# Optimization experiments

Measured on AMD Instinct MI355X. Metric: run time of the kernel, lower is better.

## Reference

```python
import jax, jax.numpy as jnp
import numpy as np

B, H, W, C = 32, 112, 112, 192
KH = KW = 3


def setup_inputs() -> dict:
    key = jax.random.key(0)
    k1, k2 = jax.random.split(key)
    x = jax.random.normal(k1, (B, H, W, C), dtype=jnp.float32)
    # depthwise kernel, HWIO with I=1 and feature_group_count=C (depth_multiplier=1)
    w = jax.random.normal(k2, (KH, KW, 1, C), dtype=jnp.float32) * 0.1
    b = jnp.zeros((C,), dtype=jnp.float32)
    return {"x": x, "w": w, "b": b}


def reference(x, w, b):
    # Depthwise conv = grouped conv with feature_group_count == channels_in.
    # stride 1, 'same' padding, dilation 1, depth_multiplier 1, linear activation.
    out = jax.lax.conv_general_dilated(
        x, w,
        window_strides=(1, 1),
        padding='SAME',
        rhs_dilation=(1, 1),
        dimension_numbers=('NHWC', 'HWIO', 'NHWC'),
        feature_group_count=C,
    )
    return out + b  # bias broadcast over channel axis
```

## Files before the change

kernel.cpp:

```cpp
#include <hip/hip_runtime.h>


constexpr int Bn = 32, Hn = 112, Wn = 112, Cn = 192, C4 = 48;
constexpr int PW = 8, PC = 8;
constexpr int WP = 14, CP = 6, HG = 4;
constexpr int NSTEP = 7;
constexpr int ROWB = 10 * PC * 16;
constexpr int GRPB = 5 * 1024;
constexpr int WLDS = 3 * GRPB;

typedef float floatx4 __attribute__((ext_vector_type(4)));

#define VMWAIT(n) asm volatile("s_waitcnt vmcnt(" #n ")" ::: "memory")

__device__ __forceinline__ floatx4 fma4(floatx4 a, floatx4 b, floatx4 c) {
  c.x = fmaf(a.x, b.x, c.x);
  c.y = fmaf(a.y, b.y, c.y);
  c.z = fmaf(a.z, b.z, c.z);
  c.w = fmaf(a.w, b.w, c.w);
  return c;
}

__global__ __launch_bounds__(128, 2) void dwconv3x3_wavepriv(
    const float* __restrict__ x,
    const float* __restrict__ wgt,
    const float* __restrict__ bias,
    float* __restrict__ out) {
  __shared__ char lds[2 * WLDS];
  const int tid = (int)threadIdx.x;
  const int lane = tid & 63;
  const int wave = tid >> 6;

  int bid = blockIdx.x;
  int chk = gridDim.x >> 3;
  int sbid = (bid & 7) * chk + (bid >> 3);
  int pid = sbid * 2 + wave;
  int cp = pid % CP;  int t1 = pid / CP;
  int wp = t1 % WP;   t1 /= WP;
  int hg = t1 & 3;    int b = t1 >> 2;

  const int hbase = hg * 28;
  const int w0 = wp * PW;
  const float* xb = x + (long)b * Hn * Wn * Cn;
  const int rstr = Wn * Cn;
  char* wl = lds + wave * WLDS;

  int rowadd[5], coloff[5];
#pragma unroll
  for (int k = 0; k < 5; ++k) {
    int q = k * 64 + lane;
    rowadd[k] = q / 80;
    int rem = q % 80;
    int col = rem >> 3, c4 = rem & 7;
    int wc = min(max(w0 + col - 1, 0), Wn - 1);
    coloff[k] = wc * Cn + cp * 32 + c4 * 4;
  }

  auto stage = [&](int g) {
    char* dst0 = wl + (g % 3) * GRPB;
#pragma unroll
    for (int k = 0; k < 5; ++k) {
      int h = min(max(hbase + 4 * g + rowadd[k] - 1, 0), Hn - 1);
      const float* src = xb + (long)h * rstr + coloff[k];
      __builtin_amdgcn_global_load_lds(
          (const __attribute__((address_space(1))) void*)src,
          (__attribute__((address_space(3))) void*)(dst0 + k * 1024),
          16, 0, 0);
    }
  };

  stage(0); stage(1); stage(2);

  const int c4i = lane & 7;
  const int wi = lane >> 3;
  const int cofs = cp * 32 + c4i * 4;
  const int wg = w0 + wi;
  const float cs0 = (wg >= 1) ? 1.f : 0.f;
  const float cs2 = (wg <= Wn - 2) ? 1.f : 0.f;
  floatx4 wv[3][3];
#pragma unroll
  for (int kh = 0; kh < 3; ++kh) {
#pragma unroll
    for (int kw = 0; kw < 3; ++kw)
      wv[kh][kw] = *(const floatx4*)(wgt + (kh * 3 + kw) * Cn + cofs);
    wv[kh][0] *= cs0;
    wv[kh][2] *= cs2;
  }
  const floatx4 bv = *(const floatx4*)(bias + cofs);
  const float sTop = (hg == 0) ? 0.f : 1.f;
  const float sBot = (hg == HG - 1) ? 0.f : 1.f;

  const int ostr = Wn * C4;
  floatx4* outp = (floatx4*)out +
      ((long)(b * Hn + hbase) * Wn + wg) * C4 + cp * PC + c4i;

#pragma unroll
  for (int t = 0; t < NSTEP; ++t) {
    if (t == 0)      VMWAIT(5);
    else if (t == 1) VMWAIT(9);
    else if (t < 6)  VMWAIT(13);
    else             VMWAIT(8);

    floatx4 acc[4];
#pragma unroll
    for (int o = 0; o < 4; ++o) acc[o] = bv;

#pragma unroll
    for (int r = 0; r < 6; ++r) {
      const int s = 4 * t + r;
      const char* base =
          wl + (s >> 2) % 3 * GRPB + (s & 3) * ROWB + 128 + lane * 16;
      floatx4 xv0 = *(const floatx4*)(base - 128);
      floatx4 xv1 = *(const floatx4*)(base);
      floatx4 xv2 = *(const floatx4*)(base + 128);
      if (t == 0 && r == 0) { xv0 *= sTop; xv1 *= sTop; xv2 *= sTop; }
      if (t == NSTEP - 1 && r == 5) { xv0 *= sBot; xv1 *= sBot; xv2 *= sBot; }
#pragma unroll
      for (int kh = 0; kh < 3; ++kh) {
        int o = r - kh;
        if (o >= 0 && o < 4) {
          acc[o] = fma4(xv0, wv[kh][0], acc[o]);
          acc[o] = fma4(xv1, wv[kh][1], acc[o]);
          acc[o] = fma4(xv2, wv[kh][2], acc[o]);
        }
      }
    }

    asm volatile("s_waitcnt lgkmcnt(0)" ::: "memory");
    __builtin_amdgcn_sched_barrier(0);
    if (t <= 4) stage(t + 3);

#pragma unroll
    for (int o = 0; o < 4; ++o)
      __builtin_nontemporal_store(acc[o], outp + (long)(4 * t + o) * ostr);
  }
}

extern "C" void kernel_launch(void* const* d_in, const int* in_sizes, int n_in,
                              void* d_out, int out_size, void* d_ws, size_t ws_size,
                              hipStream_t stream) {
  const float* x = (const float*)d_in[0];
  const float* w = (const float*)d_in[1];
  const float* b = (const float*)d_in[2];
  float* out = (float*)d_out;

  const int grid = Bn * HG * WP * CP / 2;
  dwconv3x3_wavepriv<<<grid, 128, 0, stream>>>(x, w, b, out);
}
```

Measured before the change: 107.8 us.

## Restructure depthwise conv to full-channel width-4 tiles with shared LDS pipeline

Each block of three waves now covers all 192 channels for a 4-column strip over 28 rows. It computes 2 output rows per step, where before each wave privately handled an 8-column, 32-channel patch with 4 rows per step. Rows are staged cooperatively into a 4-slot LDS ring with a block barrier, and the next stage is issued before compute instead of after it. The aim is contiguous full-row channel loads and more resident blocks (launch bounds 192,4). The trade-off is more halo overhead (6 columns loaded per 4 output columns versus 10 per 8), more rows re-read across steps, and a barrier in every step.

```diff
diff --git a/kernel.cpp b/kernel.cpp
--- a/kernel.cpp
+++ b/kernel.cpp
@@ -2,12 +2,14 @@
 
 
 constexpr int Bn = 32, Hn = 112, Wn = 112, Cn = 192, C4 = 48;
-constexpr int PW = 8, PC = 8;
-constexpr int WP = 14, CP = 6, HG = 4;
-constexpr int NSTEP = 7;
-constexpr int ROWB = 10 * PC * 16;
-constexpr int GRPB = 5 * 1024;
-constexpr int WLDS = 3 * GRPB;
+constexpr int WT = 4;
+constexpr int WTiles = Wn / WT;
+constexpr int NSTEP = 14, HG = 4;
+constexpr int LWC = 6;
+constexpr int ROWF4 = LWC * C4;
+constexpr int SLABF4 = 2 * ROWF4;
+constexpr int SLABB = SLABF4 * 16;
+constexpr int NSLOT = 4;
 
 typedef float floatx4 __attribute__((ext_vector_type(4)));
 
@@ -21,12 +23,12 @@
   return c;
 }
 
-__global__ __launch_bounds__(128, 2) void dwconv3x3_wavepriv(
+__global__ __launch_bounds__(192, 4) void dwconv3x3_dense(
     const float* __restrict__ x,
     const float* __restrict__ wgt,
     const float* __restrict__ bias,
     float* __restrict__ out) {
-  __shared__ char lds[2 * WLDS];
+  __shared__ char lds[NSLOT * SLABB];
   const int tid = (int)threadIdx.x;
   const int lane = tid & 63;
   const int wave = tid >> 6;
@@ -34,46 +36,43 @@
   int bid = blockIdx.x;
   int chk = gridDim.x >> 3;
   int sbid = (bid & 7) * chk + (bid >> 3);
-  int pid = sbid * 2 + wave;
-  int cp = pid % CP;  int t1 = pid / CP;
-  int wp = t1 % WP;   t1 /= WP;
-  int hg = t1 & 3;    int b = t1 >> 2;
+  int wt = sbid % WTiles; int tt = sbid / WTiles;
+  int hg = tt & 3;        int b = tt >> 2;
 
-  const int hbase = hg * 28;
-  const int w0 = wp * PW;
+  const int hbase = hg * (2 * NSTEP);
+  const int w0 = wt * WT;
   const float* xb = x + (long)b * Hn * Wn * Cn;
   const int rstr = Wn * Cn;
-  char* wl = lds + wave * WLDS;
 
-  int rowadd[5], coloff[5];
+  int rowadd[3], coloff[3];
 #pragma unroll
-  for (int k = 0; k < 5; ++k) {
-    int q = k * 64 + lane;
-    rowadd[k] = q / 80;
-    int rem = q % 80;
-    int col = rem >> 3, c4 = rem & 7;
+  for (int j = 0; j < 3; ++j) {
+    int q = (3 * wave + j) * 64 + lane;
+    rowadd[j] = q / ROWF4;
+    int rem = q % ROWF4;
+    int col = rem / C4, c4l = rem % C4;
     int wc = min(max(w0 + col - 1, 0), Wn - 1);
-    coloff[k] = wc * Cn + cp * 32 + c4 * 4;
+    coloff[j] = wc * Cn + c4l * 4;
   }
 
   auto stage = [&](int g) {
-    char* dst0 = wl + (g % 3) * GRPB;
+    char* slab = lds + (g & 3) * SLABB;
 #pragma unroll
-    for (int k = 0; k < 5; ++k) {
-      int h = min(max(hbase + 4 * g + rowadd[k] - 1, 0), Hn - 1);
-      const float* src = xb + (long)h * rstr + coloff[k];
+    for (int j = 0; j < 3; ++j) {
+      int h = min(max(hbase + 2 * g + rowadd[j] - 1, 0), Hn - 1);
+      const float* src = xb + (long)h * rstr + coloff[j];
       __builtin_amdgcn_global_load_lds(
           (const __attribute__((address_space(1))) void*)src,
-          (__attribute__((address_space(3))) void*)(dst0 + k * 1024),
+          (__attribute__((address_space(3))) void*)(slab + (3 * wave + j) * 1024),
           16, 0, 0);
     }
   };
 
   stage(0); stage(1); stage(2);
 
-  const int c4i = lane & 7;
-  const int wi = lane >> 3;
-  const int cofs = cp * 32 + c4i * 4;
+  const int c4i = tid % C4;
+  const int wi = tid / C4;
+  const int cofs = c4i * 4;
   const int wg = w0 + wi;
   const float cs0 = (wg >= 1) ? 1.f : 0.f;
   const float cs2 = (wg <= Wn - 2) ? 1.f : 0.f;
@@ -92,33 +91,33 @@
 
   const int ostr = Wn * C4;
   floatx4* outp = (floatx4*)out +
-      ((long)(b * Hn + hbase) * Wn + wg) * C4 + cp * PC + c4i;
+      ((long)(b * Hn + hbase) * Wn + wg) * C4 + c4i;
+  const int cbyte = (wi + 1) * (C4 * 16) + c4i * 16;
 
 #pragma unroll
   for (int t = 0; t < NSTEP; ++t) {
-    if (t == 0)      VMWAIT(5);
-    else if (t == 1) VMWAIT(9);
-    else if (t < 6)  VMWAIT(13);
-    else             VMWAIT(8);
+    if (t == 0)              VMWAIT(3);
+    else if (t == 1)         VMWAIT(5);
+    else if (t < NSTEP - 1)  VMWAIT(7);
+    else                     VMWAIT(4);
+    __builtin_amdgcn_s_barrier();
 
-    floatx4 acc[4];
+    if (t <= NSTEP - 3) stage(t + 3);
+
+    floatx4 acc[2] = {bv, bv};
 #pragma unroll
-    for (int o = 0; o < 4; ++o) acc[o] = bv;
-
+    for (int r = 0; r < 4; ++r) {
+      const int g = t + (r >> 1);
+      const char* base = lds + (g & 3) * SLABB + (r & 1) * (ROWF4 * 16) + cbyte;
+      floatx4 xv0 = *(const floatx4*)(base - 768);
+      floatx4 xv1 = *(const floatx4*)(base);
+      floatx4 xv2 = *(const floatx4*)(base + 768);
+      if (t == 0 && r == 0) { xv0 *= sTop; xv1 *= sTop; xv2 *= sTop; }
+      if (t == NSTEP - 1 && r == 3) { xv0 *= sBot; xv1 *= sBot; xv2 *= sBot; }
 #pragma unroll
-    for (int r = 0; r < 6; ++r) {
-      const int s = 4 * t + r;
-      const char* base =
-          wl + (s >> 2) % 3 * GRPB + (s & 3) * ROWB + 128 + lane * 16;
-      floatx4 xv0 = *(const floatx4*)(base - 128);
-      floatx4 xv1 = *(const floatx4*)(base);
-      floatx4 xv2 = *(const floatx4*)(base + 128);
-      if (t == 0 && r == 0) { xv0 *= sTop; xv1 *= sTop; xv2 *= sTop; }
-      if (t == NSTEP - 1 && r == 5) { xv0 *= sBot; xv1 *= sBot; xv2 *= sBot; }
-#pragma unroll
-      for (int kh = 0; kh < 3; ++kh) {
-        int o = r - kh;
-        if (o >= 0 && o < 4) {
+      for (int o = 0; o < 2; ++o) {
+        int kh = r - o;
+        if (kh >= 0 && kh < 3) {
           acc[o] = fma4(xv0, wv[kh][0], acc[o]);
           acc[o] = fma4(xv1, wv[kh][1], acc[o]);
           acc[o] = fma4(xv2, wv[kh][2], acc[o]);
@@ -126,13 +125,9 @@
       }
     }
 
-    asm volatile("s_waitcnt lgkmcnt(0)" ::: "memory");
-    __builtin_amdgcn_sched_barrier(0);
-    if (t <= 4) stage(t + 3);
-
 #pragma unroll
-    for (int o = 0; o < 4; ++o)
-      __builtin_nontemporal_store(acc[o], outp + (long)(4 * t + o) * ostr);
+    for (int o = 0; o < 2; ++o)
+      __builtin_nontemporal_store(acc[o], outp + (long)(2 * t + o) * ostr);
   }
 }
 
@@ -144,6 +139,6 @@
   const float* b = (const float*)d_in[2];
   float* out = (float*)d_out;
 
-  const int grid = Bn * HG * WP * CP / 2;
-  dwconv3x3_wavepriv<<<grid, 128, 0, stream>>>(x, w, b, out);
+  const int grid = Bn * HG * WTiles;
+  dwconv3x3_dense<<<grid, 192, 0, stream>>>(x, w, b, out);
 }
```

Result: slower. 110.8 us (+2.8%).
